# Kernel tuning notes

Hardware: AMD Instinct MI355X
Metric: run time of the kernel (lower is better)

## Reference

```python
import jax, jax.numpy as jnp
import numpy as np

EPS = 1e-5  # torch LayerNorm default

def ln(x, g, b):
    mu = jnp.mean(x, axis=-1, keepdims=True)
    var = jnp.mean((x - mu) ** 2, axis=-1, keepdims=True)
    return (x - mu) * jax.lax.rsqrt(var + EPS) * g + b

B, S, E, A = 131072, 199, 3, 32
D_IN = S + 1  # state_dim + 1 (time feature)

def setup_inputs() -> dict:
    key = jax.random.key(0)
    ks = iter(jax.random.split(key, 32))
    def w(shape, fan_in):
        lim = 1.0 / np.sqrt(fan_in)
        return jax.random.uniform(next(ks), shape, jnp.float32, -lim, lim)
    inp = {
        "state": jax.random.normal(next(ks), (B, S), jnp.float32),
        "time_delta": jax.random.uniform(next(ks), (B,), jnp.float32),
        # trunk: Linear(200,256)+LN, Linear(256,256)+LN, Linear(256,128)+LN
        "W1": w((D_IN, 256), D_IN), "b1": w((256,), D_IN),
        "g1": jnp.ones((256,), jnp.float32), "be1": jnp.zeros((256,), jnp.float32),
        "W2": w((256, 256), 256), "b2": w((256,), 256),
        "g2": jnp.ones((256,), jnp.float32), "be2": jnp.zeros((256,), jnp.float32),
        "W3": w((256, 128), 256), "b3": w((128,), 256),
        "g3": jnp.ones((128,), jnp.float32), "be3": jnp.zeros((128,), jnp.float32),
        # value stream
        "Wv1": w((128, 64), 128), "bv1": w((64,), 128),
        "gv": jnp.ones((64,), jnp.float32), "bev": jnp.zeros((64,), jnp.float32),
        "Wv2": w((64, 1), 64), "bv2": w((1,), 64),
        # E stacked advantage streams (all heads share action dim A)
        "Wa1": w((E, 128, 64), 128), "ba1": w((E, 64), 128),
        "ga": jnp.ones((E, 64), jnp.float32), "bea": jnp.zeros((E, 64), jnp.float32),
        "Wa2": w((E, 64, A), 64), "ba2": w((E, A), 64),
        "event_type": jax.random.randint(next(ks), (B,), 0, E),
    }
    return inp

def reference(state, time_delta,
              W1, b1, g1, be1, W2, b2, g2, be2, W3, b3, g3, be3,
              Wv1, bv1, gv, bev, Wv2, bv2,
              Wa1, ba1, ga, bea, Wa2, ba2, event_type):
    td = time_delta[:, None]                       # [B,1]
    x = jnp.concatenate([state, td], axis=1)       # [B,200]
    h = jax.nn.relu(ln(x @ W1 + b1, g1, be1))      # [B,256]
    h = jax.nn.relu(ln(h @ W2 + b2, g2, be2))      # [B,256]
    f = jax.nn.relu(ln(h @ W3 + b3, g3, be3))      # [B,128]
    v = jax.nn.relu(ln(f @ Wv1 + bv1, gv, bev)) @ Wv2 + bv2  # [B,1]
    # compute all E advantage heads, then per-sample select by event_type
    h1 = jnp.einsum('bd,edh->ebh', f, Wa1) + ba1[:, None, :]           # [E,B,64]
    h1 = jax.nn.relu(ln(h1, ga[:, None, :], bea[:, None, :]))
    adv_all = jnp.einsum('ebh,eha->eba', h1, Wa2) + ba2[:, None, :]    # [E,B,A]
    adv = jnp.take_along_axis(adv_all, event_type[None, :, None], axis=0)[0]  # [B,A]
    return v + (adv - adv.mean(axis=1, keepdims=True))
```

## Files before the change

### kernel.cpp

```cpp
#include <hip/hip_runtime.h>
#include <hip/hip_bf16.h>
#include <stdint.h>

#define DEV __device__ __forceinline__

typedef __attribute__((ext_vector_type(8))) short short8;
typedef __attribute__((ext_vector_type(4))) float floatx4;

constexpr int TM  = 64;
constexpr int NB  = 131072;
constexpr int AST = 264;

constexpr int OFF_W1 = 0;
constexpr int OFF_W2 = 57344;
constexpr int OFF_W3 = 122880;
constexpr int OFF_WH = 155648;
constexpr int OFF_WA2= 188416;
constexpr int NWQ    = 194560;

constexpr int C_B1=0, C_G1=256, C_BE1=512, C_B2=768, C_G2=1024, C_BE2=1280,
  C_B3=1536, C_G3=1664, C_BE3=1792, C_BV1=1920, C_GV=1984, C_BEV=2048,
  C_WV2=2112, C_BV2=2176, C_BA1=2177, C_GA=2369, C_BEA=2561, C_BA2=2753;
constexpr int NCONST=2849;

struct Ptrs {
  const float *state,*td,*W1,*b1,*g1,*be1,*W2,*b2,*g2,*be2,*W3,*b3,*g3,*be3,
    *Wv1,*bv1,*gv,*bev,*Wv2,*bv2,*Wa1,*ba1,*ga,*bea,*Wa2,*ba2;
  const int *et;
};

DEV unsigned short f2bf(float x){
  uint32_t u = __float_as_uint(x);
  u += 0x7fffu + ((u>>16)&1u);
  return (unsigned short)(u>>16);
}
DEV uint32_t f2bf_pk(float a, float b){
  float2 f2; f2.x=a; f2.y=b;
  __hip_bfloat162 h = __float22bfloat162_rn(f2);
  union { __hip_bfloat162 h; uint32_t u; } cv; cv.h = h;
  return cv.u;
}

__global__ void prep_kernel(Ptrs p, unsigned short* __restrict__ wq, float* __restrict__ cq){
  int idx = blockIdx.x*256 + threadIdx.x;
  if (idx < NWQ) {
    float v = 0.f;
    if (idx < OFF_W2) {
      int e = idx, w = e/14336, r = e%14336;
      int kc = r>>11, ct=(r>>9)&3, l=(r>>3)&63, j=r&7;
      int n = w*64 + ct*16 + (l&15);
      int k = kc*32 + (l>>4)*8 + j;
      if (k < 200) v = p.W1[k*256 + n];
    } else if (idx < OFF_W3) {
      int e = idx-OFF_W2, w=e>>14, r=e&16383;
      int kc=r>>11, ct=(r>>9)&3, l=(r>>3)&63, j=r&7;
      int n = w*64 + ct*16 + (l&15);
      int k = kc*32 + (l>>4)*8 + j;
      int c = (k & ~63) + 16*(k&3) + ((k&63)>>2);
      v = p.W2[c*256 + n];
    } else if (idx < OFF_WH) {
      int e = idx-OFF_W3, w=e>>13, r=e&8191;
      int kc=r>>10, ct=(r>>9)&1, l=(r>>3)&63, j=r&7;
      int n = w*32 + ct*16 + (l&15);
      int k = kc*32 + (l>>4)*8 + j;
      int c = (k & ~63) + 16*(k&3) + ((k&63)>>2);
      v = p.W3[c*128 + n];
    } else if (idx < OFF_WA2) {
      int e = idx-OFF_WH, h=e>>13, r=e&8191;
      int kc=r>>11, ct=(r>>9)&3, l=(r>>3)&63, j=r&7;
      int n = ct*16 + (l&15);
      int k = kc*32 + (l>>4)*8 + j;
      int c = (k & ~31) + 16*(k&1) + ((k&31)>>1);
      v = (h<3) ? p.Wa1[h*8192 + c*64 + n] : p.Wv1[c*64 + n];
    } else {
      int e = idx-OFF_WA2, h=e>>11, r=e&2047;
      int kc=r>>10, ct=(r>>9)&1, l=(r>>3)&63, j=r&7;
      int n = ct*16 + (l&15);
      int k = kc*32 + (l>>4)*8 + j;
      int c = 16*(k&3) + (k>>2);
      v = p.Wa2[h*2048 + c*32 + n];
    }
    wq[idx] = f2bf(v);
  } else if (idx < NWQ + NCONST) {
    int ci = idx - NWQ;
    const float* src; int off;
    if      (ci < 256)  { src=p.b1;  off=ci; }
    else if (ci < 512)  { src=p.g1;  off=ci-256; }
    else if (ci < 768)  { src=p.be1; off=ci-512; }
    else if (ci < 1024) { src=p.b2;  off=ci-768; }
    else if (ci < 1280) { src=p.g2;  off=ci-1024; }
    else if (ci < 1536) { src=p.be2; off=ci-1280; }
    else if (ci < 1664) { src=p.b3;  off=ci-1536; }
    else if (ci < 1792) { src=p.g3;  off=ci-1664; }
    else if (ci < 1920) { src=p.be3; off=ci-1792; }
    else if (ci < 1984) { src=p.bv1; off=ci-1920; }
    else if (ci < 2048) { src=p.gv;  off=ci-1984; }
    else if (ci < 2112) { src=p.bev; off=ci-2048; }
    else if (ci < 2176) { src=p.Wv2; off=ci-2112; }
    else if (ci < 2177) { src=p.bv2; off=ci-2176; }
    else if (ci < 2369) { src=p.ba1; off=ci-2177; }
    else if (ci < 2561) { src=p.ga;  off=ci-2369; }
    else if (ci < 2753) { src=p.bea; off=ci-2561; }
    else                { src=p.ba2; off=ci-2753; }
    cq[ci] = src[off];
  }
}

template<int N>
DEV void loadB(short8 (&B)[N], const unsigned short* __restrict__ src, int lane){
  #pragma unroll
  for (int i=0;i<N;i++) B[i] = *(const short8*)(src + i*512 + lane*8);
}

template<int CT>
DEV void zeroAcc(floatx4 (&acc)[4][4]){
  const floatx4 z = {0.f,0.f,0.f,0.f};
  #pragma unroll
  for (int rt=0;rt<4;rt++)
    #pragma unroll
    for (int ct=0;ct<CT;ct++) acc[rt][ct]=z;
}

template<int KC,int CT>
DEV void runGemm(floatx4 (&acc)[4][4], const short8 (&B)[KC*CT],
                 const unsigned short* aBase, int aOff){
  #pragma unroll
  for (int kc=0;kc<KC;kc++){
    short8 a[4];
    #pragma unroll
    for (int rt=0;rt<4;rt++)
      a[rt] = *(const short8*)(aBase + rt*16*AST + aOff + kc*32);
    #pragma unroll
    for (int rt=0;rt<4;rt++)
      #pragma unroll
      for (int ct=0;ct<CT;ct++)
        acc[rt][ct] = __builtin_amdgcn_mfma_f32_16x16x32_bf16(a[rt], B[kc*CT+ct], acc[rt][ct], 0,0,0);
  }
}

template<int CT>
DEV void biasStatsWrite(floatx4 (&acc)[4][4], const float* __restrict__ cq, int bo, int colBase,
                        float2* pstatw, int ln, int q){
  float bias[CT];
  #pragma unroll
  for (int ct=0;ct<CT;ct++) bias[ct]=cq[bo+colBase+ct*16+ln];
  #pragma unroll
  for (int rt=0;rt<4;rt++){
    float s[4]={0,0,0,0}, ss[4]={0,0,0,0};
    #pragma unroll
    for (int ct=0;ct<CT;ct++){
      #pragma unroll
      for (int r=0;r<4;r++){
        float v=acc[rt][ct][r]+bias[ct];
        acc[rt][ct][r]=v; s[r]+=v; ss[r]+=v*v;
      }
    }
    #pragma unroll
    for (int r=0;r<4;r++){
      #pragma unroll
      for (int d=1;d<16;d<<=1){ s[r]+=__shfl_xor(s[r],d); ss[r]+=__shfl_xor(ss[r],d); }
      if (ln==0) pstatw[rt*16+q*4+r] = make_float2(s[r], ss[r]);
    }
  }
}

template<int CT>
DEV void lnWrite(floatx4 (&acc)[4][4], const float* __restrict__ cq, int go, int beo, int colBase,
                 const float2* fstat, unsigned short* act_, int ln, int q){
  float g[CT], be[CT];
  #pragma unroll
  for (int ct=0;ct<CT;ct++){ g[ct]=cq[go+colBase+ct*16+ln]; be[ct]=cq[beo+colBase+ct*16+ln]; }
  #pragma unroll
  for (int rt=0;rt<4;rt++){
    #pragma unroll
    for (int r=0;r<4;r++){
      int row=rt*16+q*4+r;
      float2 st=fstat[row];
      unsigned short* pp = act_ + row*AST + colBase + ln*CT;
      float y[CT];
      #pragma unroll
      for (int ct=0;ct<CT;ct++)
        y[ct] = fmaxf((acc[rt][ct][r]-st.x)*st.y*g[ct]+be[ct], 0.f);
      if constexpr (CT==4){
        uint2 pk; pk.x = f2bf_pk(y[0],y[1]); pk.y = f2bf_pk(y[2],y[3]);
        *(uint2*)pp = pk;
      } else {
        *(uint32_t*)pp = f2bf_pk(y[0],y[1]);
      }
    }
  }
}

__global__ __launch_bounds__(256,3) void dqn_main(
    const float* __restrict__ state, const float* __restrict__ td,
    const int* __restrict__ et, const unsigned short* __restrict__ wq,
    const float* __restrict__ cq, float* __restrict__ out)
{
  __shared__ __align__(16) unsigned short act[TM*AST];
  __shared__ float2 pstat[4*64];
  __shared__ float2 fstat[64];
  __shared__ float  advbuf[64*32];
  __shared__ float  vbuf[64];
  __shared__ int    etl[64];

  const int tid=threadIdx.x, w=tid>>6, lane=tid&63, q=lane>>4, ln=lane&15;
  const int rowBlk = blockIdx.x*TM;

  {
    const float* sbase = state + (size_t)rowBlk*199;
    for (int i=tid; i<64*199; i+=256){
      float v = sbase[i];
      int row = i/199, col = i - row*199;
      act[row*AST+col] = f2bf(v);
    }
    for (int i=tid; i<64*25; i+=256){
      int row = i/25, c = 199 + (i - row*25);
      unsigned short hv = 0;
      if (c==199) hv = f2bf(td[rowBlk+row]);
      act[row*AST+c] = hv;
    }
    if (tid < 64) etl[tid] = et[rowBlk+tid];
  }
  __syncthreads();

  const unsigned short* aBase = act + ln*AST + q*8;
  floatx4 acc[4][4];

  {
    short8 B[28];
    loadB<28>(B, wq + OFF_W1 + w*14336, lane);
    zeroAcc<4>(acc);
    runGemm<7,4>(acc, B, aBase, 0);
  }
  biasStatsWrite<4>(acc, cq, C_B1, w*64, &pstat[w*64], ln, q);
  __syncthreads();
  if (tid<64){
    float s=0, ss=0;
    #pragma unroll
    for (int ww=0;ww<4;ww++){ float2 pp=pstat[ww*64+tid]; s+=pp.x; ss+=pp.y; }
    float mu=s*(1.f/256.f), var=ss*(1.f/256.f)-mu*mu;
    fstat[tid]=make_float2(mu, rsqrtf(var+1e-5f));
  }
  __syncthreads();
  lnWrite<4>(acc, cq, C_G1, C_BE1, w*64, fstat, act, ln, q);
  __syncthreads();

  {
    short8 B[32];
    loadB<32>(B, wq + OFF_W2 + w*16384, lane);
    zeroAcc<4>(acc);
    runGemm<8,4>(acc, B, aBase, 0);
  }
  biasStatsWrite<4>(acc, cq, C_B2, w*64, &pstat[w*64], ln, q);
  __syncthreads();
  if (tid<64){
    float s=0, ss=0;
    #pragma unroll
    for (int ww=0;ww<4;ww++){ float2 pp=pstat[ww*64+tid]; s+=pp.x; ss+=pp.y; }
    float mu=s*(1.f/256.f), var=ss*(1.f/256.f)-mu*mu;
    fstat[tid]=make_float2(mu, rsqrtf(var+1e-5f));
  }
  __syncthreads();
  lnWrite<4>(acc, cq, C_G2, C_BE2, w*64, fstat, act, ln, q);
  __syncthreads();

  {
    short8 B[16];
    loadB<16>(B, wq + OFF_W3 + w*8192, lane);
    zeroAcc<2>(acc);
    runGemm<8,2>(acc, B, aBase, 0);
  }
  biasStatsWrite<2>(acc, cq, C_B3, w*32, &pstat[w*64], ln, q);
  __syncthreads();
  if (tid<64){
    float s=0, ss=0;
    #pragma unroll
    for (int ww=0;ww<4;ww++){ float2 pp=pstat[ww*64+tid]; s+=pp.x; ss+=pp.y; }
    float mu=s*(1.f/128.f), var=ss*(1.f/128.f)-mu*mu;
    fstat[tid]=make_float2(mu, rsqrtf(var+1e-5f));
  }
  __syncthreads();
  lnWrite<2>(acc, cq, C_G3, C_BE3, w*32, fstat, act, ln, q);
  __syncthreads();

  {
    short8 B[16];
    loadB<16>(B, wq + OFF_WH + w*8192, lane);
    zeroAcc<4>(acc);
    runGemm<4,4>(acc, B, aBase, 0);
  }
  {
    const int bo = (w<3)? C_BA1+w*64 : C_BV1;
    const int go = (w<3)? C_GA +w*64 : C_GV;
    const int beo= (w<3)? C_BEA+w*64 : C_BEV;
    float bias[4], g[4], be[4];
    #pragma unroll
    for (int ct=0;ct<4;ct++){ bias[ct]=cq[bo+ct*16+ln]; g[ct]=cq[go+ct*16+ln]; be[ct]=cq[beo+ct*16+ln]; }
    #pragma unroll
    for (int rt=0;rt<4;rt++){
      float s[4]={0,0,0,0}, ss[4]={0,0,0,0};
      #pragma unroll
      for (int ct=0;ct<4;ct++)
        #pragma unroll
        for (int r=0;r<4;r++){
          float v=acc[rt][ct][r]+bias[ct];
          acc[rt][ct][r]=v; s[r]+=v; ss[r]+=v*v;
        }
      float mu[4], rs[4];
      #pragma unroll
      for (int r=0;r<4;r++){
        #pragma unroll
        for (int d=1;d<16;d<<=1){ s[r]+=__shfl_xor(s[r],d); ss[r]+=__shfl_xor(ss[r],d); }
        mu[r]=s[r]*(1.f/64.f);
        rs[r]=rsqrtf(ss[r]*(1.f/64.f)-mu[r]*mu[r]+1e-5f);
      }
      #pragma unroll
      for (int ct=0;ct<4;ct++)
        #pragma unroll
        for (int r=0;r<4;r++)
          acc[rt][ct][r]=fmaxf((acc[rt][ct][r]-mu[r])*rs[r]*g[ct]+be[ct], 0.f);
    }
  }

  if (w==3){
    float wv[4];
    #pragma unroll
    for (int ct=0;ct<4;ct++) wv[ct]=cq[C_WV2+ct*16+ln];
    float bv2v = cq[C_BV2];
    #pragma unroll
    for (int rt=0;rt<4;rt++){
      float dd[4]={0,0,0,0};
      #pragma unroll
      for (int ct=0;ct<4;ct++)
        #pragma unroll
        for (int r=0;r<4;r++) dd[r]+=acc[rt][ct][r]*wv[ct];
      #pragma unroll
      for (int r=0;r<4;r++){
        #pragma unroll
        for (int d=1;d<16;d<<=1) dd[r]+=__shfl_xor(dd[r],d);
        if (ln==0) vbuf[rt*16+q*4+r]=dd[r]+bv2v;
      }
    }
  }
  __syncthreads();

  if (w<3){
    #pragma unroll
    for (int rt=0;rt<4;rt++)
      #pragma unroll
      for (int r=0;r<4;r++){
        int row=rt*16+q*4+r;
        unsigned short* pp = act + row*AST + 64*w + ln*4;
        uint2 pk;
        pk.x = f2bf_pk(acc[rt][0][r], acc[rt][1][r]);
        pk.y = f2bf_pk(acc[rt][2][r], acc[rt][3][r]);
        *(uint2*)pp = pk;
      }
    short8 B2[4];
    loadB<4>(B2, wq + OFF_WA2 + w*2048, lane);
    zeroAcc<2>(acc);
    runGemm<2,2>(acc, B2, aBase, 64*w);
    #pragma unroll
    for (int ct=0;ct<2;ct++){
      float b2v = cq[C_BA2 + w*32 + ct*16 + ln];
      #pragma unroll
      for (int rt=0;rt<4;rt++)
        #pragma unroll
        for (int r=0;r<4;r++){
          int row=rt*16+q*4+r;
          if (etl[row]==w) advbuf[row*32 + ct*16 + ln] = acc[rt][ct][r] + b2v;
        }
    }
  }
  __syncthreads();

  if (tid<64){
    float s=0;
    #pragma unroll
    for (int cc=0;cc<32;cc++){ int c=(cc+tid)&31; s+=advbuf[tid*32+c]; }
    fstat[tid].x = s*(1.f/32.f);
  }
  __syncthreads();
  {
    int row = tid>>2, c0=(tid&3)*8;
    float v = vbuf[row], m = fstat[row].x;
    float4 o0, o1;
    o0.x = v + advbuf[row*32+c0+0] - m;  o0.y = v + advbuf[row*32+c0+1] - m;
    o0.z = v + advbuf[row*32+c0+2] - m;  o0.w = v + advbuf[row*32+c0+3] - m;
    o1.x = v + advbuf[row*32+c0+4] - m;  o1.y = v + advbuf[row*32+c0+5] - m;
    o1.z = v + advbuf[row*32+c0+6] - m;  o1.w = v + advbuf[row*32+c0+7] - m;
    float* op = out + (size_t)(rowBlk+row)*32 + c0;
    *(float4*)op = o0;
    *(float4*)(op+4) = o1;
  }
}

extern "C" void kernel_launch(void* const* d_in, const int* in_sizes, int n_in,
                              void* d_out, int out_size, void* d_ws, size_t ws_size,
                              hipStream_t stream)
{
  Ptrs p;
  p.state=(const float*)d_in[0];  p.td =(const float*)d_in[1];
  p.W1 =(const float*)d_in[2];  p.b1 =(const float*)d_in[3];  p.g1 =(const float*)d_in[4];  p.be1=(const float*)d_in[5];
  p.W2 =(const float*)d_in[6];  p.b2 =(const float*)d_in[7];  p.g2 =(const float*)d_in[8];  p.be2=(const float*)d_in[9];
  p.W3 =(const float*)d_in[10]; p.b3 =(const float*)d_in[11]; p.g3 =(const float*)d_in[12]; p.be3=(const float*)d_in[13];
  p.Wv1=(const float*)d_in[14]; p.bv1=(const float*)d_in[15]; p.gv =(const float*)d_in[16]; p.bev=(const float*)d_in[17];
  p.Wv2=(const float*)d_in[18]; p.bv2=(const float*)d_in[19];
  p.Wa1=(const float*)d_in[20]; p.ba1=(const float*)d_in[21]; p.ga =(const float*)d_in[22]; p.bea=(const float*)d_in[23];
  p.Wa2=(const float*)d_in[24]; p.ba2=(const float*)d_in[25];
  p.et =(const int*)d_in[26];

  unsigned short* wq = (unsigned short*)d_ws;
  float* cq = (float*)((char*)d_ws + (size_t)NWQ*2);

  const int prepN = NWQ + NCONST;
  hipLaunchKernelGGL(prep_kernel, dim3((prepN+255)/256), dim3(256), 0, stream, p, wq, cq);
  hipLaunchKernelGGL(dqn_main, dim3(NB/TM), dim3(256), 0, stream,
                     p.state, p.td, p.et, (const unsigned short*)wq, (const float*)cq, (float*)d_out);
}
```

Measured before the change: 320.3 us.

## Double-buffer weight slices across GEMM stages and fold layer-1 bias into padding

Replaces the bulk per-layer load of all weight fragments into registers with a two-slot register double buffer. The next K-chunk is prefetched while the current one is multiplied, and the first slice of each following layer is loaded before the LayerNorm/sync phases. The layer-1 bias moves into the padded K column (weight row 200 times an activation of 1.0). Bias addition is deferred into the LN write, and the head epilogue writes directly without a separate pass. The aim is lower register pressure (from up to 32 short8 down to 8), better occupancy, and weight-load latency hidden behind compute and barriers. The cost is more interleaved loads inside the MFMA loop.

```diff
diff --git a/kernel.cpp b/kernel.cpp
--- a/kernel.cpp
+++ b/kernel.cpp
@@ -51,6 +51,7 @@
       int n = w*64 + ct*16 + (l&15);
       int k = kc*32 + (l>>4)*8 + j;
       if (k < 200) v = p.W1[k*256 + n];
+      else if (k == 200) v = p.b1[n];
     } else if (idx < OFF_W3) {
       int e = idx-OFF_W2, w=e>>14, r=e&16383;
       int kc=r>>11, ct=(r>>9)&3, l=(r>>3)&63, j=r&7;
@@ -106,10 +107,10 @@
   }
 }
 
-template<int N>
-DEV void loadB(short8 (&B)[N], const unsigned short* __restrict__ src, int lane){
-  #pragma unroll
-  for (int i=0;i<N;i++) B[i] = *(const short8*)(src + i*512 + lane*8);
+template<int CT>
+DEV void loadBslice(short8* Bb, const unsigned short* __restrict__ src, int lane){
+  #pragma unroll
+  for (int ct=0;ct<CT;ct++) Bb[ct] = *(const short8*)(src + ct*512 + lane*8);
 }
 
 template<int CT>
@@ -122,10 +123,14 @@
 }
 
 template<int KC,int CT>
-DEV void runGemm(floatx4 (&acc)[4][4], const short8 (&B)[KC*CT],
-                 const unsigned short* aBase, int aOff){
+DEV void gemmPipe(floatx4 (&acc)[4][4], short8 (&Ba)[4], short8 (&Bbuf)[4],
+                  const unsigned short* __restrict__ wsrc,
+                  const unsigned short* aBase, int aOff, int lane){
   #pragma unroll
   for (int kc=0;kc<KC;kc++){
+    short8* cur = (kc&1)? Bbuf : Ba;
+    short8* nxt = (kc&1)? Ba   : Bbuf;
+    if (kc+1<KC) loadBslice<CT>(nxt, wsrc + (kc+1)*CT*512, lane);
     short8 a[4];
     #pragma unroll
     for (int rt=0;rt<4;rt++)
@@ -134,16 +139,20 @@
     for (int rt=0;rt<4;rt++)
       #pragma unroll
       for (int ct=0;ct<CT;ct++)
-        acc[rt][ct] = __builtin_amdgcn_mfma_f32_16x16x32_bf16(a[rt], B[kc*CT+ct], acc[rt][ct], 0,0,0);
-  }
-}
-
-template<int CT>
-DEV void biasStatsWrite(floatx4 (&acc)[4][4], const float* __restrict__ cq, int bo, int colBase,
-                        float2* pstatw, int ln, int q){
-  float bias[CT];
-  #pragma unroll
-  for (int ct=0;ct<CT;ct++) bias[ct]=cq[bo+colBase+ct*16+ln];
+        acc[rt][ct] = __builtin_amdgcn_mfma_f32_16x16x32_bf16(a[rt], cur[ct], acc[rt][ct], 0,0,0);
+  }
+}
+
+template<int CT,bool BIAS>
+DEV void statsPhase(const floatx4 (&acc)[4][4], const float* __restrict__ cq, int bo, int colBase,
+                    float2* pstatw, int ln, int q, float (&bias)[4]){
+  if constexpr (BIAS){
+    #pragma unroll
+    for (int ct=0;ct<CT;ct++) bias[ct]=cq[bo+colBase+ct*16+ln];
+  } else {
+    #pragma unroll
+    for (int ct=0;ct<CT;ct++) bias[ct]=0.f;
+  }
   #pragma unroll
   for (int rt=0;rt<4;rt++){
     float s[4]={0,0,0,0}, ss[4]={0,0,0,0};
@@ -152,7 +161,7 @@
       #pragma unroll
       for (int r=0;r<4;r++){
         float v=acc[rt][ct][r]+bias[ct];
-        acc[rt][ct][r]=v; s[r]+=v; ss[r]+=v*v;
+        s[r]+=v; ss[r]+=v*v;
       }
     }
     #pragma unroll
@@ -165,8 +174,8 @@
 }
 
 template<int CT>
-DEV void lnWrite(floatx4 (&acc)[4][4], const float* __restrict__ cq, int go, int beo, int colBase,
-                 const float2* fstat, unsigned short* act_, int ln, int q){
+DEV void lnWrite(const floatx4 (&acc)[4][4], const float* __restrict__ cq, int go, int beo, int colBase,
+                 const float2* fstat, unsigned short* act_, int ln, int q, const float (&bias)[4]){
   float g[CT], be[CT];
   #pragma unroll
   for (int ct=0;ct<CT;ct++){ g[ct]=cq[go+colBase+ct*16+ln]; be[ct]=cq[beo+colBase+ct*16+ln]; }
@@ -180,7 +189,7 @@
       float y[CT];
       #pragma unroll
       for (int ct=0;ct<CT;ct++)
-        y[ct] = fmaxf((acc[rt][ct][r]-st.x)*st.y*g[ct]+be[ct], 0.f);
+        y[ct] = fmaxf((acc[rt][ct][r]+bias[ct]-st.x)*st.y*g[ct]+be[ct], 0.f);
       if constexpr (CT==4){
         uint2 pk; pk.x = f2bf_pk(y[0],y[1]); pk.y = f2bf_pk(y[2],y[3]);
         *(uint2*)pp = pk;
@@ -188,6 +197,16 @@
         *(uint32_t*)pp = f2bf_pk(y[0],y[1]);
       }
     }
+  }
+}
+
+DEV void fstatReduce(const float2* pstat, float2* fstat, int tid, float invN){
+  if (tid<64){
+    float s=0, ss=0;
+    #pragma unroll
+    for (int ww=0;ww<4;ww++){ float2 pp=pstat[ww*64+tid]; s+=pp.x; ss+=pp.y; }
+    float mu=s*invN, var=ss*invN-mu*mu;
+    fstat[tid]=make_float2(mu, rsqrtf(var+1e-5f));
   }
 }
 
@@ -206,6 +225,15 @@
   const int tid=threadIdx.x, w=tid>>6, lane=tid&63, q=lane>>4, ln=lane&15;
   const int rowBlk = blockIdx.x*TM;
 
+  const unsigned short* wqL1 = wq + OFF_W1 + w*14336;
+  const unsigned short* wqL2 = wq + OFF_W2 + w*16384;
+  const unsigned short* wqL3 = wq + OFF_W3 + w*8192;
+  const unsigned short* wqH  = wq + OFF_WH + w*8192;
+  const unsigned short* wqA2 = wq + OFF_WA2 + w*2048;
+
+  short8 Ba[4], Bbuf[4];
+  loadBslice<4>(Ba, wqL1, lane);
+
   {
     const float* sbase = state + (size_t)rowBlk*199;
     for (int i=tid; i<64*199; i+=256){
@@ -217,6 +245,7 @@
       int row = i/25, c = 199 + (i - row*25);
       unsigned short hv = 0;
       if (c==199) hv = f2bf(td[rowBlk+row]);
+      else if (c==200) hv = 0x3F80u;
       act[row*AST+c] = hv;
     }
     if (tid < 64) etl[tid] = et[rowBlk+tid];
@@ -225,86 +254,64 @@
 
   const unsigned short* aBase = act + ln*AST + q*8;
   floatx4 acc[4][4];
-
-  {
-    short8 B[28];
-    loadB<28>(B, wq + OFF_W1 + w*14336, lane);
-    zeroAcc<4>(acc);
-    runGemm<7,4>(acc, B, aBase, 0);
-  }
-  biasStatsWrite<4>(acc, cq, C_B1, w*64, &pstat[w*64], ln, q);
-  __syncthreads();
-  if (tid<64){
-    float s=0, ss=0;
-    #pragma unroll
-    for (int ww=0;ww<4;ww++){ float2 pp=pstat[ww*64+tid]; s+=pp.x; ss+=pp.y; }
-    float mu=s*(1.f/256.f), var=ss*(1.f/256.f)-mu*mu;
-    fstat[tid]=make_float2(mu, rsqrtf(var+1e-5f));
-  }
-  __syncthreads();
-  lnWrite<4>(acc, cq, C_G1, C_BE1, w*64, fstat, act, ln, q);
-  __syncthreads();
-
-  {
-    short8 B[32];
-    loadB<32>(B, wq + OFF_W2 + w*16384, lane);
-    zeroAcc<4>(acc);
-    runGemm<8,4>(acc, B, aBase, 0);
-  }
-  biasStatsWrite<4>(acc, cq, C_B2, w*64, &pstat[w*64], ln, q);
-  __syncthreads();
-  if (tid<64){
-    float s=0, ss=0;
-    #pragma unroll
-    for (int ww=0;ww<4;ww++){ float2 pp=pstat[ww*64+tid]; s+=pp.x; ss+=pp.y; }
-    float mu=s*(1.f/256.f), var=ss*(1.f/256.f)-mu*mu;
-    fstat[tid]=make_float2(mu, rsqrtf(var+1e-5f));
-  }
-  __syncthreads();
-  lnWrite<4>(acc, cq, C_G2, C_BE2, w*64, fstat, act, ln, q);
-  __syncthreads();
-
-  {
-    short8 B[16];
-    loadB<16>(B, wq + OFF_W3 + w*8192, lane);
-    zeroAcc<2>(acc);
-    runGemm<8,2>(acc, B, aBase, 0);
-  }
-  biasStatsWrite<2>(acc, cq, C_B3, w*32, &pstat[w*64], ln, q);
-  __syncthreads();
-  if (tid<64){
-    float s=0, ss=0;
-    #pragma unroll
-    for (int ww=0;ww<4;ww++){ float2 pp=pstat[ww*64+tid]; s+=pp.x; ss+=pp.y; }
-    float mu=s*(1.f/128.f), var=ss*(1.f/128.f)-mu*mu;
-    fstat[tid]=make_float2(mu, rsqrtf(var+1e-5f));
-  }
-  __syncthreads();
-  lnWrite<2>(acc, cq, C_G3, C_BE3, w*32, fstat, act, ln, q);
-  __syncthreads();
-
-  {
-    short8 B[16];
-    loadB<16>(B, wq + OFF_WH + w*8192, lane);
-    zeroAcc<4>(acc);
-    runGemm<4,4>(acc, B, aBase, 0);
-  }
+  float bias[4];
+
+  zeroAcc<4>(acc);
+  gemmPipe<7,4>(acc, Ba, Bbuf, wqL1, aBase, 0, lane);
+  loadBslice<4>(Ba, wqL2, lane);
+  statsPhase<4,false>(acc, cq, 0, w*64, &pstat[w*64], ln, q, bias);
+  __syncthreads();
+  fstatReduce(pstat, fstat, tid, 1.f/256.f);
+  __syncthreads();
+  lnWrite<4>(acc, cq, C_G1, C_BE1, w*64, fstat, act, ln, q, bias);
+  __syncthreads();
+
+  zeroAcc<4>(acc);
+  gemmPipe<8,4>(acc, Ba, Bbuf, wqL2, aBase, 0, lane);
+  loadBslice<2>(Ba, wqL3, lane);
+  statsPhase<4,true>(acc, cq, C_B2, w*64, &pstat[w*64], ln, q, bias);
+  __syncthreads();
+  fstatReduce(pstat, fstat, tid, 1.f/256.f);
+  __syncthreads();
+  lnWrite<4>(acc, cq, C_G2, C_BE2, w*64, fstat, act, ln, q, bias);
+  __syncthreads();
+
+  zeroAcc<2>(acc);
+  gemmPipe<8,2>(acc, Ba, Bbuf, wqL3, aBase, 0, lane);
+  loadBslice<4>(Ba, wqH, lane);
+  statsPhase<2,true>(acc, cq, C_B3, w*32, &pstat[w*64], ln, q, bias);
+  __syncthreads();
+  fstatReduce(pstat, fstat, tid, 1.f/128.f);
+  __syncthreads();
+  lnWrite<2>(acc, cq, C_G3, C_BE3, w*32, fstat, act, ln, q, bias);
+  __syncthreads();
+
+  zeroAcc<4>(acc);
+  gemmPipe<4,4>(acc, Ba, Bbuf, wqH, aBase, 0, lane);
+  if (w<3) loadBslice<2>(Ba, wqA2, lane);
   {
     const int bo = (w<3)? C_BA1+w*64 : C_BV1;
     const int go = (w<3)? C_GA +w*64 : C_GV;
     const int beo= (w<3)? C_BEA+w*64 : C_BEV;
-    float bias[4], g[4], be[4];
-    #pragma unroll
-    for (int ct=0;ct<4;ct++){ bias[ct]=cq[bo+ct*16+ln]; g[ct]=cq[go+ct*16+ln]; be[ct]=cq[beo+ct*16+ln]; }
+    float bi[4], g[4], be[4];
+    #pragma unroll
+    for (int ct=0;ct<4;ct++){ bi[ct]=cq[bo+ct*16+ln]; g[ct]=cq[go+ct*16+ln]; be[ct]=cq[beo+ct*16+ln]; }
+    float wv[4]; float bv2v = 0.f;
+    if (w==3){
+      #pragma unroll
+      for (int ct=0;ct<4;ct++) wv[ct]=cq[C_WV2+ct*16+ln];
+      bv2v = cq[C_BV2];
+    }
     #pragma unroll
     for (int rt=0;rt<4;rt++){
+      float y[4][4];
       float s[4]={0,0,0,0}, ss[4]={0,0,0,0};
       #pragma unroll
       for (int ct=0;ct<4;ct++)
         #pragma unroll
         for (int r=0;r<4;r++){
-          float v=acc[rt][ct][r]+bias[ct];
-          acc[rt][ct][r]=v; s[r]+=v; ss[r]+=v*v;
+          float v=acc[rt][ct][r]+bi[ct];
+          y[ct][r]=v; s[r]+=v; ss[r]+=v*v;
         }
       float mu[4], rs[4];
       #pragma unroll
@@ -318,48 +325,38 @@
       for (int ct=0;ct<4;ct++)
         #pragma unroll
         for (int r=0;r<4;r++)
-          acc[rt][ct][r]=fmaxf((acc[rt][ct][r]-mu[r])*rs[r]*g[ct]+be[ct], 0.f);
-    }
-  }
-
-  if (w==3){
-    float wv[4];
-    #pragma unroll
-    for (int ct=0;ct<4;ct++) wv[ct]=cq[C_WV2+ct*16+ln];
-    float bv2v = cq[C_BV2];
-    #pragma unroll
-    for (int rt=0;rt<4;rt++){
-      float dd[4]={0,0,0,0};
-      #pragma unroll
-      for (int ct=0;ct<4;ct++)
-        #pragma unroll
-        for (int r=0;r<4;r++) dd[r]+=acc[rt][ct][r]*wv[ct];
-      #pragma unroll
-      for (int r=0;r<4;r++){
-        #pragma unroll
-        for (int d=1;d<16;d<<=1) dd[r]+=__shfl_xor(dd[r],d);
-        if (ln==0) vbuf[rt*16+q*4+r]=dd[r]+bv2v;
+          y[ct][r]=fmaxf((y[ct][r]-mu[r])*rs[r]*g[ct]+be[ct], 0.f);
+
+      if (w==3){
+        float dd[4]={0,0,0,0};
+        #pragma unroll
+        for (int ct=0;ct<4;ct++)
+          #pragma unroll
+          for (int r=0;r<4;r++) dd[r]+=y[ct][r]*wv[ct];
+        #pragma unroll
+        for (int r=0;r<4;r++){
+          #pragma unroll
+          for (int d=1;d<16;d<<=1) dd[r]+=__shfl_xor(dd[r],d);
+          if (ln==0) vbuf[rt*16+q*4+r]=dd[r]+bv2v;
+        }
+      } else {
+        #pragma unroll
+        for (int r=0;r<4;r++){
+          int row=rt*16+q*4+r;
+          unsigned short* pp = act + row*AST + 64*w + ln*4;
+          uint2 pk;
+          pk.x = f2bf_pk(y[0][r], y[1][r]);
+          pk.y = f2bf_pk(y[2][r], y[3][r]);
+          *(uint2*)pp = pk;
+        }
       }
     }
   }
   __syncthreads();
 
   if (w<3){
-    #pragma unroll
-    for (int rt=0;rt<4;rt++)
-      #pragma unroll
-      for (int r=0;r<4;r++){
-        int row=rt*16+q*4+r;
-        unsigned short* pp = act + row*AST + 64*w + ln*4;
-        uint2 pk;
-        pk.x = f2bf_pk(acc[rt][0][r], acc[rt][1][r]);
-        pk.y = f2bf_pk(acc[rt][2][r], acc[rt][3][r]);
-        *(uint2*)pp = pk;
-      }
-    short8 B2[4];
-    loadB<4>(B2, wq + OFF_WA2 + w*2048, lane);
     zeroAcc<2>(acc);
-    runGemm<2,2>(acc, B2, aBase, 64*w);
+    gemmPipe<2,2>(acc, Ba, Bbuf, wqA2, aBase, 64*w, lane);
     #pragma unroll
     for (int ct=0;ct<2;ct++){
       float b2v = cq[C_BA2 + w*32 + ct*16 + ln];
```

After: 316.6 us. Within noise of the previous version (-1.2%).

## Replace LayerNorm stat reduction passes with LDS atomics and fold bias into GEMM

Applied to the files above, without the earlier changes.

Row statistics for each LayerNorm are now accumulated with shared-memory atomicAdd into double-buffered sum arrays, and every thread computes mean and rstd itself. This removes one barrier and the single-wave reduction step per layer. The first-layer bias is folded into the GEMM through a constant-one input column and matching weight row. The advantage mean is computed with shuffles and written straight to global memory, which drops advbuf, two barriers and a staging pass. Launch bounds rise to four blocks per CU, which may increase register pressure or spilling, and the scattered per-lane global writes may coalesce less well than the old float4 stores.

```diff
diff --git a/kernel.cpp b/kernel.cpp
--- a/kernel.cpp
+++ b/kernel.cpp
@@ -51,6 +51,7 @@
       int n = w*64 + ct*16 + (l&15);
       int k = kc*32 + (l>>4)*8 + j;
       if (k < 200) v = p.W1[k*256 + n];
+      else if (k == 200) v = p.b1[n];
     } else if (idx < OFF_W3) {
       int e = idx-OFF_W2, w=e>>14, r=e&16383;
       int kc=r>>11, ct=(r>>9)&3, l=(r>>3)&63, j=r&7;
@@ -138,12 +139,11 @@
   }
 }
 
-template<int CT>
-DEV void biasStatsWrite(floatx4 (&acc)[4][4], const float* __restrict__ cq, int bo, int colBase,
-                        float2* pstatw, int ln, int q){
-  float bias[CT];
-  #pragma unroll
-  for (int ct=0;ct<CT;ct++) bias[ct]=cq[bo+colBase+ct*16+ln];
+template<int CT,bool BIAS>
+DEV void statsAtomic(const floatx4 (&acc)[4][4], const float* __restrict__ cq, int bo, int colBase,
+                     float* sbuf, float* ssbuf, int ln, int q, float (&bias)[4]){
+  #pragma unroll
+  for (int ct=0;ct<CT;ct++) bias[ct] = BIAS ? cq[bo+colBase+ct*16+ln] : 0.f;
   #pragma unroll
   for (int rt=0;rt<4;rt++){
     float s[4]={0,0,0,0}, ss[4]={0,0,0,0};
@@ -152,35 +152,43 @@
       #pragma unroll
       for (int r=0;r<4;r++){
         float v=acc[rt][ct][r]+bias[ct];
-        acc[rt][ct][r]=v; s[r]+=v; ss[r]+=v*v;
+        s[r]+=v; ss[r]+=v*v;
       }
     }
     #pragma unroll
     for (int r=0;r<4;r++){
       #pragma unroll
       for (int d=1;d<16;d<<=1){ s[r]+=__shfl_xor(s[r],d); ss[r]+=__shfl_xor(ss[r],d); }
-      if (ln==0) pstatw[rt*16+q*4+r] = make_float2(s[r], ss[r]);
+      if (ln==0){
+        int row = rt*16+q*4+r;
+        atomicAdd(&sbuf[row],  s[r]);
+        atomicAdd(&ssbuf[row], ss[r]);
+      }
     }
   }
 }
 
 template<int CT>
-DEV void lnWrite(floatx4 (&acc)[4][4], const float* __restrict__ cq, int go, int beo, int colBase,
-                 const float2* fstat, unsigned short* act_, int ln, int q){
+DEV void lnWrite(const floatx4 (&acc)[4][4], const float* __restrict__ cq, int go, int beo, int colBase,
+                 const float* sbuf, const float* ssbuf, float invN,
+                 unsigned short* act_, int ln, int q, const float (&bias)[4]){
   float g[CT], be[CT];
   #pragma unroll
   for (int ct=0;ct<CT;ct++){ g[ct]=cq[go+colBase+ct*16+ln]; be[ct]=cq[beo+colBase+ct*16+ln]; }
   #pragma unroll
   for (int rt=0;rt<4;rt++){
+    floatx4 sv  = *(const floatx4*)&sbuf [rt*16+q*4];
+    floatx4 ssv = *(const floatx4*)&ssbuf[rt*16+q*4];
     #pragma unroll
     for (int r=0;r<4;r++){
+      float mu = sv[r]*invN;
+      float rs = rsqrtf(ssv[r]*invN - mu*mu + 1e-5f);
       int row=rt*16+q*4+r;
-      float2 st=fstat[row];
       unsigned short* pp = act_ + row*AST + colBase + ln*CT;
       float y[CT];
       #pragma unroll
       for (int ct=0;ct<CT;ct++)
-        y[ct] = fmaxf((acc[rt][ct][r]-st.x)*st.y*g[ct]+be[ct], 0.f);
+        y[ct] = fmaxf((acc[rt][ct][r]+bias[ct]-mu)*rs*g[ct]+be[ct], 0.f);
       if constexpr (CT==4){
         uint2 pk; pk.x = f2bf_pk(y[0],y[1]); pk.y = f2bf_pk(y[2],y[3]);
         *(uint2*)pp = pk;
@@ -191,32 +199,32 @@
   }
 }
 
-__global__ __launch_bounds__(256,3) void dqn_main(
+__global__ __launch_bounds__(256,4) void dqn_main(
     const float* __restrict__ state, const float* __restrict__ td,
     const int* __restrict__ et, const unsigned short* __restrict__ wq,
     const float* __restrict__ cq, float* __restrict__ out)
 {
   __shared__ __align__(16) unsigned short act[TM*AST];
-  __shared__ float2 pstat[4*64];
-  __shared__ float2 fstat[64];
-  __shared__ float  advbuf[64*32];
-  __shared__ float  vbuf[64];
-  __shared__ int    etl[64];
+  __shared__ float sstat[2][2][64];
+  __shared__ float vbuf[64];
+  __shared__ int   etl[64];
 
   const int tid=threadIdx.x, w=tid>>6, lane=tid&63, q=lane>>4, ln=lane&15;
   const int rowBlk = blockIdx.x*TM;
 
   {
+    ((float*)sstat)[tid] = 0.f;
     const float* sbase = state + (size_t)rowBlk*199;
     for (int i=tid; i<64*199; i+=256){
       float v = sbase[i];
       int row = i/199, col = i - row*199;
       act[row*AST+col] = f2bf(v);
     }
-    for (int i=tid; i<64*25; i+=256){
-      int row = i/25, c = 199 + (i - row*25);
+    for (int i=tid; i<64*32; i+=256){
+      int row = i>>5, c = 199 + (i&31);
       unsigned short hv = 0;
       if (c==199) hv = f2bf(td[rowBlk+row]);
+      else if (c==200) hv = 0x3F80u;
       act[row*AST+c] = hv;
     }
     if (tid < 64) etl[tid] = et[rowBlk+tid];
@@ -225,6 +233,7 @@
 
   const unsigned short* aBase = act + ln*AST + q*8;
   floatx4 acc[4][4];
+  float bias[4];
 
   {
     short8 B[28];
@@ -232,17 +241,9 @@
     zeroAcc<4>(acc);
     runGemm<7,4>(acc, B, aBase, 0);
   }
-  biasStatsWrite<4>(acc, cq, C_B1, w*64, &pstat[w*64], ln, q);
-  __syncthreads();
-  if (tid<64){
-    float s=0, ss=0;
-    #pragma unroll
-    for (int ww=0;ww<4;ww++){ float2 pp=pstat[ww*64+tid]; s+=pp.x; ss+=pp.y; }
-    float mu=s*(1.f/256.f), var=ss*(1.f/256.f)-mu*mu;
-    fstat[tid]=make_float2(mu, rsqrtf(var+1e-5f));
-  }
-  __syncthreads();
-  lnWrite<4>(acc, cq, C_G1, C_BE1, w*64, fstat, act, ln, q);
+  statsAtomic<4,false>(acc, cq, 0, w*64, sstat[0][0], sstat[0][1], ln, q, bias);
+  __syncthreads();
+  lnWrite<4>(acc, cq, C_G1, C_BE1, w*64, sstat[0][0], sstat[0][1], 1.f/256.f, act, ln, q, bias);
   __syncthreads();
 
   {
@@ -251,17 +252,10 @@
     zeroAcc<4>(acc);
     runGemm<8,4>(acc, B, aBase, 0);
   }
-  biasStatsWrite<4>(acc, cq, C_B2, w*64, &pstat[w*64], ln, q);
-  __syncthreads();
-  if (tid<64){
-    float s=0, ss=0;
-    #pragma unroll
-    for (int ww=0;ww<4;ww++){ float2 pp=pstat[ww*64+tid]; s+=pp.x; ss+=pp.y; }
-    float mu=s*(1.f/256.f), var=ss*(1.f/256.f)-mu*mu;
-    fstat[tid]=make_float2(mu, rsqrtf(var+1e-5f));
-  }
-  __syncthreads();
-  lnWrite<4>(acc, cq, C_G2, C_BE2, w*64, fstat, act, ln, q);
+  statsAtomic<4,true>(acc, cq, C_B2, w*64, sstat[1][0], sstat[1][1], ln, q, bias);
+  __syncthreads();
+  if (tid < 128) ((float*)sstat[0])[tid] = 0.f;
+  lnWrite<4>(acc, cq, C_G2, C_BE2, w*64, sstat[1][0], sstat[1][1], 1.f/256.f, act, ln, q, bias);
   __syncthreads();
 
   {
@@ -270,17 +264,9 @@
     zeroAcc<2>(acc);
     runGemm<8,2>(acc, B, aBase, 0);
   }
-  biasStatsWrite<2>(acc, cq, C_B3, w*32, &pstat[w*64], ln, q);
-  __syncthreads();
-  if (tid<64){
-    float s=0, ss=0;
-    #pragma unroll
-    for (int ww=0;ww<4;ww++){ float2 pp=pstat[ww*64+tid]; s+=pp.x; ss+=pp.y; }
-    float mu=s*(1.f/128.f), var=ss*(1.f/128.f)-mu*mu;
-    fstat[tid]=make_float2(mu, rsqrtf(var+1e-5f));
-  }
-  __syncthreads();
-  lnWrite<2>(acc, cq, C_G3, C_BE3, w*32, fstat, act, ln, q);
+  statsAtomic<2,true>(acc, cq, C_B3, w*32, sstat[0][0], sstat[0][1], ln, q, bias);
+  __syncthreads();
+  lnWrite<2>(acc, cq, C_G3, C_BE3, w*32, sstat[0][0], sstat[0][1], 1.f/128.f, act, ln, q, bias);
   __syncthreads();
 
   {
@@ -293,52 +279,61 @@
     const int bo = (w<3)? C_BA1+w*64 : C_BV1;
     const int go = (w<3)? C_GA +w*64 : C_GV;
     const int beo= (w<3)? C_BEA+w*64 : C_BEV;
-    float bias[4], g[4], be[4];
-    #pragma unroll
-    for (int ct=0;ct<4;ct++){ bias[ct]=cq[bo+ct*16+ln]; g[ct]=cq[go+ct*16+ln]; be[ct]=cq[beo+ct*16+ln]; }
+    float bi[4], g[4], be[4];
+    #pragma unroll
+    for (int ct=0;ct<4;ct++){ bi[ct]=cq[bo+ct*16+ln]; g[ct]=cq[go+ct*16+ln]; be[ct]=cq[beo+ct*16+ln]; }
+    float wv[4]; float bv2v = 0.f;
+    if (w==3){
+      #pragma unroll
+      for (int ct=0;ct<4;ct++) wv[ct]=cq[C_WV2+ct*16+ln];
+      bv2v = cq[C_BV2];
+    }
     #pragma unroll
     for (int rt=0;rt<4;rt++){
+      float y[4][4];
       float s[4]={0,0,0,0}, ss[4]={0,0,0,0};
       #pragma unroll
       for (int ct=0;ct<4;ct++)
         #pragma unroll
         for (int r=0;r<4;r++){
-          float v=acc[rt][ct][r]+bias[ct];
-          acc[rt][ct][r]=v; s[r]+=v; ss[r]+=v*v;
+          float v=acc[rt][ct][r]+bi[ct];
+          y[ct][r]=v; s[r]+=v; ss[r]+=v*v;
         }
-      float mu[4], rs[4];
       #pragma unroll
       for (int r=0;r<4;r++){
         #pragma unroll
         for (int d=1;d<16;d<<=1){ s[r]+=__shfl_xor(s[r],d); ss[r]+=__shfl_xor(ss[r],d); }
-        mu[r]=s[r]*(1.f/64.f);
-        rs[r]=rsqrtf(ss[r]*(1.f/64.f)-mu[r]*mu[r]+1e-5f);
-      }
-      #pragma unroll
-      for (int ct=0;ct<4;ct++)
-        #pragma unroll
-        for (int r=0;r<4;r++)
-          acc[rt][ct][r]=fmaxf((acc[rt][ct][r]-mu[r])*rs[r]*g[ct]+be[ct], 0.f);
-    }
-  }
-
-  if (w==3){
-    float wv[4];
-    #pragma unroll
-    for (int ct=0;ct<4;ct++) wv[ct]=cq[C_WV2+ct*16+ln];
-    float bv2v = cq[C_BV2];
-    #pragma unroll
-    for (int rt=0;rt<4;rt++){
-      float dd[4]={0,0,0,0};
-      #pragma unroll
-      for (int ct=0;ct<4;ct++)
-        #pragma unroll
-        for (int r=0;r<4;r++) dd[r]+=acc[rt][ct][r]*wv[ct];
-      #pragma unroll
-      for (int r=0;r<4;r++){
-        #pragma unroll
-        for (int d=1;d<16;d<<=1) dd[r]+=__shfl_xor(dd[r],d);
-        if (ln==0) vbuf[rt*16+q*4+r]=dd[r]+bv2v;
+        float mu=s[r]*(1.f/64.f);
+        float rs=rsqrtf(ss[r]*(1.f/64.f)-mu*mu+1e-5f);
+        #pragma unroll
+        for (int ct=0;ct<4;ct++)
+          y[ct][r]=fmaxf((y[ct][r]-mu)*rs*g[ct]+be[ct], 0.f);
+      }
+
+      if (w==3){
+        float dd[4]={0,0,0,0};
+        #pragma unroll
+        for (int ct=0;ct<4;ct++)
+          #pragma unroll
+          for (int r=0;r<4;r++) dd[r]+=y[ct][r]*wv[ct];
+        #pragma unroll
+        for (int r=0;r<4;r++){
+          #pragma unroll
+          for (int d=1;d<16;d<<=1) dd[r]+=__shfl_xor(dd[r],d);
+          if (ln==0) vbuf[rt*16+q*4+r]=dd[r]+bv2v;
+        }
+      } else {
+        #pragma unroll
+        for (int r=0;r<4;r++){
+          int row=rt*16+q*4+r;
+          (void)row;
+        }
+      }
+      if (w<3){
+        #pragma unroll
+        for (int ct=0;ct<4;ct++)
+          #pragma unroll
+          for (int r=0;r<4;r++) acc[rt][ct][r]=y[ct][r];
       }
     }
   }
@@ -360,38 +355,26 @@
     loadB<4>(B2, wq + OFF_WA2 + w*2048, lane);
     zeroAcc<2>(acc);
     runGemm<2,2>(acc, B2, aBase, 64*w);
-    #pragma unroll
-    for (int ct=0;ct<2;ct++){
-      float b2v = cq[C_BA2 + w*32 + ct*16 + ln];
-      #pragma unroll
-      for (int rt=0;rt<4;rt++)
-        #pragma unroll
-        for (int r=0;r<4;r++){
-          int row=rt*16+q*4+r;
-          if (etl[row]==w) advbuf[row*32 + ct*16 + ln] = acc[rt][ct][r] + b2v;
+    float b20 = cq[C_BA2 + w*32 + ln];
+    float b21 = cq[C_BA2 + w*32 + 16 + ln];
+    #pragma unroll
+    for (int rt=0;rt<4;rt++)
+      #pragma unroll
+      for (int r=0;r<4;r++){
+        float a0 = acc[rt][0][r] + b20;
+        float a1 = acc[rt][1][r] + b21;
+        float sm = a0 + a1;
+        #pragma unroll
+        for (int d=1;d<16;d<<=1) sm += __shfl_xor(sm,d);
+        int row = rt*16+q*4+r;
+        if (etl[row]==w){
+          float vv = vbuf[row];
+          float m  = sm*(1.f/32.f);
+          float* op = out + (size_t)(rowBlk+row)*32 + ln;
+          op[0]  = vv + a0 - m;
+          op[16] = vv + a1 - m;
         }
-    }
-  }
-  __syncthreads();
-
-  if (tid<64){
-    float s=0;
-    #pragma unroll
-    for (int cc=0;cc<32;cc++){ int c=(cc+tid)&31; s+=advbuf[tid*32+c]; }
-    fstat[tid].x = s*(1.f/32.f);
-  }
-  __syncthreads();
-  {
-    int row = tid>>2, c0=(tid&3)*8;
-    float v = vbuf[row], m = fstat[row].x;
-    float4 o0, o1;
-    o0.x = v + advbuf[row*32+c0+0] - m;  o0.y = v + advbuf[row*32+c0+1] - m;
-    o0.z = v + advbuf[row*32+c0+2] - m;  o0.w = v + advbuf[row*32+c0+3] - m;
-    o1.x = v + advbuf[row*32+c0+4] - m;  o1.y = v + advbuf[row*32+c0+5] - m;
-    o1.z = v + advbuf[row*32+c0+6] - m;  o1.w = v + advbuf[row*32+c0+7] - m;
-    float* op = out + (size_t)(rowBlk+row)*32 + c0;
-    *(float4*)op = o0;
-    *(float4*)(op+4) = o1;
+      }
   }
 }
 
```

New measurement: 310.2 us. 1.03x faster.
